# Optimization experiments

Measured on AMD Instinct MI355X. Metric: run time of the kernel, lower is better.

## Reference

```python
import jax, jax.numpy as jnp
import numpy as np

B, S, H = 2, 2048, 2048
NH, NKV, HD = 16, 4, 128
LAT = H // 8  # compression_ratio=8


def _rope_tables():
    inv_freq = 1.0 / (10000.0 ** (jnp.arange(0, HD, 2, dtype=jnp.float32) / HD))
    pos = jnp.arange(S, dtype=jnp.float32)
    freqs = pos[:, None] * inv_freq[None, :]          # [S, HD/2]
    emb = jnp.concatenate([freqs, freqs], axis=-1)    # [S, HD]
    return jnp.cos(emb)[None, None], jnp.sin(emb)[None, None]  # [1,1,S,HD]


def setup_inputs() -> dict:
    key = jax.random.key(0)
    ks = jax.random.split(key, 8)
    std = 0.02
    hidden_states = jax.random.normal(ks[0], (B, S, H), dtype=jnp.float32)
    cos, sin = _rope_tables()
    # additive causal mask, broadcast over batch/heads
    causal = jnp.tril(jnp.ones((S, S), dtype=bool))
    attention_mask = jnp.where(causal, 0.0, -1e9).astype(jnp.float32)[None, None]
    Wq = jax.random.normal(ks[1], (H, H), dtype=jnp.float32) * std
    Wk = jax.random.normal(ks[2], (NKV * HD, H), dtype=jnp.float32) * std
    Wv = jax.random.normal(ks[3], (NKV * HD, H), dtype=jnp.float32) * std
    Wo = jax.random.normal(ks[4], (H, H), dtype=jnp.float32) * std
    Wl_in = jax.random.normal(ks[5], (LAT, H), dtype=jnp.float32) * std
    Wl_out = jax.random.normal(ks[6], (H, LAT), dtype=jnp.float32) * std
    latent_gate = jnp.ones((1,), dtype=jnp.float32)
    return dict(hidden_states=hidden_states, cos=cos, sin=sin,
                attention_mask=attention_mask, Wq=Wq, Wk=Wk, Wv=Wv, Wo=Wo,
                Wl_in=Wl_in, Wl_out=Wl_out, latent_gate=latent_gate)


def _rotate_half(x):
    x1, x2 = jnp.split(x, 2, axis=-1)
    return jnp.concatenate([-x2, x1], axis=-1)


def reference(hidden_states, cos, sin, attention_mask, Wq, Wk, Wv, Wo,
              Wl_in, Wl_out, latent_gate):
    b, s, h = hidden_states.shape
    # projections (torch Linear: x @ W.T)
    q = (hidden_states @ Wq.T).reshape(b, s, NH, HD).transpose(0, 2, 1, 3)    # [b,nh,s,hd]
    k = (hidden_states @ Wk.T).reshape(b, s, NKV, HD).transpose(0, 2, 1, 3)   # [b,nkv,s,hd]
    v = (hidden_states @ Wv.T).reshape(b, s, NKV, HD).transpose(0, 2, 1, 3)
    # inline RoPE
    c, sn = cos[:, :, :s, :], sin[:, :, :s, :]
    q = q * c + _rotate_half(q) * sn
    k = k * c + _rotate_half(k) * sn
    # GQA: replicate kv heads (repeat_interleave along head dim)
    rep = NH // NKV
    k = jnp.repeat(k, rep, axis=1)
    v = jnp.repeat(v, rep, axis=1)
    scores = jnp.einsum('bhqd,bhkd->bhqk', q, k) / np.sqrt(HD).astype(np.float32)
    scores = scores + attention_mask
    attn = jax.nn.softmax(scores, axis=-1)
    ctx = jnp.einsum('bhqk,bhkd->bhqd', attn, v)          # [b,nh,s,hd]
    ctx = ctx.transpose(0, 2, 1, 3).reshape(b, s, h)
    attn_out = ctx @ Wo.T
    latent = (hidden_states @ Wl_in.T) @ Wl_out.T          # low-rank residual branch
    return attn_out + latent_gate * latent
```

## Files before the change

### kernel.cpp

```cpp
#include <hip/hip_runtime.h>
#include <hip/hip_bf16.h>

#define Bn   2
#define Sn   2048
#define Hn   2048
#define NHn  16
#define NKVn 4
#define HDn  128
#define LATn 256
#define Mn   (Bn*Sn)
#define KC   2304
#define NWn  3328

typedef unsigned short ushort_t;
typedef __attribute__((ext_vector_type(8))) short bf16x8;
typedef __attribute__((ext_vector_type(8))) unsigned short ushort8;
typedef __attribute__((ext_vector_type(4))) float f32x4;
typedef __attribute__((ext_vector_type(4))) unsigned u32x4;

__device__ __forceinline__ ushort_t f2bf(float f) {
    unsigned u = __float_as_uint(f);
    u += 0x7fffu + ((u >> 16) & 1u);
    return (ushort_t)(u >> 16);
}
__device__ __forceinline__ float bf2f(ushort_t h) {
    return __uint_as_float(((unsigned)h) << 16);
}
__device__ __forceinline__ unsigned cvt_pk_bf16(float lo, float hi) {
    unsigned r;
    asm("v_cvt_pk_bf16_f32 %0, %1, %2" : "=v"(r) : "v"(lo), "v"(hi));
    return r;
}
__device__ __forceinline__ void async16(const void* g, void* l) {
    __builtin_amdgcn_global_load_lds(
        (__attribute__((address_space(1))) void*)g,
        (__attribute__((address_space(3))) void*)l, 16, 0, 0);
}

struct CastArgs {
    const float* src[7];
    ushort_t*    dst[7];
    int n4[7];
    int sshift[7];
    int dcols[7];
    int dcoff[7];
};
__global__ __launch_bounds__(256)
void cast_fused(CastArgs a)
{
    int off = blockIdx.x * 256 + threadIdx.x;
    int seg = 0;
    while (seg < 6 && off >= a.n4[seg]) { off -= a.n4[seg]; ++seg; }
    const int r = off >> a.sshift[seg];
    const int c = off & ((1 << a.sshift[seg]) - 1);
    float4 f = ((const float4*)a.src[seg])[off];
    ushort4 o;
    o.x = f2bf(f.x); o.y = f2bf(f.y); o.z = f2bf(f.z); o.w = f2bf(f.w);
    ((ushort4*)a.dst[seg])[(size_t)r * a.dcols[seg] + a.dcoff[seg] + c] = o;
}

#define GEMM_BK64_LOOP(Aptr, Astr, Wptr, Wstr, Kdim)                          \
    for (int k0 = 0; k0 < (Kdim); k0 += 64) {                                 \
        _Pragma("unroll")                                                     \
        for (int it = 0; it < 4; ++it)                                        \
            async16((Aptr) + (size_t)(m0 + it*32 + srow)*(Astr) + k0 + scol,  \
                    As + (it*256 + tid)*8);                                   \
        _Pragma("unroll")                                                     \
        for (int it = 0; it < 4; ++it)                                        \
            async16((Wptr) + (size_t)(n0 + it*32 + srow)*(Wstr) + k0 + scol,  \
                    Bsm + (it*256 + tid)*8);                                  \
        __syncthreads();                                                      \
        _Pragma("unroll")                                                     \
        for (int hf = 0; hf < 2; ++hf) {                                      \
            bf16x8 af[4], bfr[4];                                             \
            _Pragma("unroll")                                                 \
            for (int mi = 0; mi < 4; ++mi)                                    \
                af[mi] = *(const bf16x8*)(As + aoff[hf*4 + mi]);              \
            _Pragma("unroll")                                                 \
            for (int ni = 0; ni < 4; ++ni)                                    \
                bfr[ni] = *(const bf16x8*)(Bsm + boff[hf*4 + ni]);            \
            _Pragma("unroll")                                                 \
            for (int mi = 0; mi < 4; ++mi)                                    \
                _Pragma("unroll")                                             \
                for (int ni = 0; ni < 4; ++ni)                                \
                    acc[mi][ni] = __builtin_amdgcn_mfma_f32_16x16x32_bf16(    \
                        af[mi], bfr[ni], acc[mi][ni], 0, 0, 0);               \
        }                                                                     \
        __syncthreads();                                                      \
    }

#define GEMM_COMMON_DECLS                                                     \
    const int tid  = threadIdx.x;                                             \
    const int lane = tid & 63, w = tid >> 6;                                  \
    const int t = lane & 15, q = lane >> 4;                                   \
    const int wm = w & 1, wn = w >> 1;                                        \
    const int srow = tid >> 3;                                                \
    const int scol = ((tid & 7) ^ ((tid >> 3) & 7)) * 8;                      \
    int aoff[8], boff[8];                                                     \
    _Pragma("unroll")                                                         \
    for (int hf = 0; hf < 2; ++hf)                                            \
        _Pragma("unroll")                                                     \
        for (int i = 0; i < 4; ++i) {                                         \
            aoff[hf*4 + i] = (wm*64 + i*16 + t)*64 + (((hf*4 + q) ^ (t & 7)) << 3); \
            boff[hf*4 + i] = (wn*64 + i*16 + t)*64 + (((hf*4 + q) ^ (t & 7)) << 3); \
        }                                                                     \
    f32x4 acc[4][4];                                                          \
    _Pragma("unroll")                                                         \
    for (int i = 0; i < 4; ++i)                                               \
        _Pragma("unroll")                                                     \
        for (int j = 0; j < 4; ++j) acc[i][j] = (f32x4){0.f, 0.f, 0.f, 0.f};

__global__ __launch_bounds__(256, 4)
void gemm_qkv(const ushort_t* __restrict__ A, const ushort_t* __restrict__ W,
              ushort_t* __restrict__ qo, ushort_t* __restrict__ ko,
              ushort_t* __restrict__ vo, ushort_t* __restrict__ ctxb,
              const float* __restrict__ gatep,
              const float* __restrict__ cosb, const float* __restrict__ sinb)
{
    __shared__ __align__(16) ushort_t smem[16384];
    ushort_t* As  = smem;
    ushort_t* Bsm = smem + 8192;

    const int m0 = blockIdx.y * 128, n0 = blockIdx.x * 128;
    GEMM_COMMON_DECLS
    GEMM_BK64_LOOP(A, Hn, W, Hn, Hn)

    const int bidx = m0 >> 11, s0 = m0 & (Sn - 1);

    if (n0 >= 2560 && n0 < 3072) {
        const int head = (n0 - 2560) >> 7;
        ushort_t* T = smem;
        #pragma unroll
        for (int h2 = 0; h2 < 2; ++h2) {
            __syncthreads();
            if (wn == h2) {
                #pragma unroll
                for (int mi = 0; mi < 4; ++mi)
                    #pragma unroll
                    for (int ni = 0; ni < 4; ++ni)
                        #pragma unroll
                        for (int r = 0; r < 4; ++r)
                            T[(wm*64 + mi*16 + q*4 + r)*64 + ni*16 + t] =
                                f2bf(acc[mi][ni][r]);
            }
            __syncthreads();
            const int dl = tid >> 2, tseg = (tid & 3) * 32;
            const size_t base =
                ((size_t)(bidx*NKVn + head)*HDn + h2*64 + dl) * Sn + s0 + tseg;
            #pragma unroll
            for (int j0 = 0; j0 < 4; ++j0) {
                ushort8 pk;
                #pragma unroll
                for (int u = 0; u < 8; ++u) {
                    const int p  = j0*8 + u;
                    const int qg = (p >> 3) & 3, j = p & 7;
                    const int orig = (j < 4) ? qg*4 + j : 16 + qg*4 + (j - 4);
                    pk[u] = T[(tseg + orig)*64 + dl];
                }
                *(ushort8*)(vo + base + j0*8) = pk;
            }
        }
        return;
    }

    if (n0 >= 3072) {
        const float gate = gatep[0];
        ushort_t* obase = ctxb + (size_t)m0 * KC + (2048 + (n0 - 3072));
        #pragma unroll
        for (int mi = 0; mi < 4; ++mi)
            #pragma unroll
            for (int r = 0; r < 4; ++r) {
                const int sl = wm*64 + mi*16 + q*4 + r;
                #pragma unroll
                for (int ni = 0; ni < 4; ++ni) {
                    const int d = wn*64 + ni*16 + t;
                    obase[(size_t)sl*KC + d] = f2bf(gate * acc[mi][ni][r]);
                }
            }
        return;
    }

    ushort_t* obase;
    float qsc;
    if (n0 < 2048) {
        obase = qo + (((size_t)(bidx*NHn + (n0 >> 7)))*Sn + s0) * HDn;
        qsc = 0.12751744737492532f;
    } else {
        obase = ko + (((size_t)(bidx*NKVn + ((n0 - 2048) >> 7)))*Sn + s0) * HDn;
        qsc = 1.0f;
    }

    float* smf = (float*)smem;
    if (wn == 1) {
        #pragma unroll
        for (int mi = 0; mi < 4; ++mi)
            #pragma unroll
            for (int r = 0; r < 4; ++r) {
                const int sl = wm*64 + mi*16 + q*4 + r;
                #pragma unroll
                for (int ni = 0; ni < 4; ++ni)
                    smf[sl*64 + (((ni*16 + t) ^ (((sl >> 2) & 3) << 4)))] =
                        acc[mi][ni][r];
            }
    }
    __syncthreads();
    if (wn == 0) {
        #pragma unroll
        for (int mi = 0; mi < 4; ++mi)
            #pragma unroll
            for (int r = 0; r < 4; ++r) {
                const int sl = wm*64 + mi*16 + q*4 + r;
                const int s  = s0 + sl;
                #pragma unroll
                for (int ni = 0; ni < 4; ++ni) {
                    const int d = ni*16 + t;
                    const float c  = cosb[s*HDn + d];
                    const float sn = sinb[s*HDn + d];
                    const float x0 = acc[mi][ni][r];
                    const float x1 = smf[sl*64 + (d ^ (((sl >> 2) & 3) << 4))];
                    obase[(size_t)sl*HDn + d] = f2bf(qsc*(x0*c - x1*sn));
                }
            }
    }
    __syncthreads();
    if (wn == 0) {
        #pragma unroll
        for (int mi = 0; mi < 4; ++mi)
            #pragma unroll
            for (int r = 0; r < 4; ++r) {
                const int sl = wm*64 + mi*16 + q*4 + r;
                #pragma unroll
                for (int ni = 0; ni < 4; ++ni)
                    smf[sl*64 + (((ni*16 + t) ^ (((sl >> 2) & 3) << 4)))] =
                        acc[mi][ni][r];
            }
    }
    __syncthreads();
    if (wn == 1) {
        #pragma unroll
        for (int mi = 0; mi < 4; ++mi)
            #pragma unroll
            for (int r = 0; r < 4; ++r) {
                const int sl = wm*64 + mi*16 + q*4 + r;
                const int s  = s0 + sl;
                #pragma unroll
                for (int ni = 0; ni < 4; ++ni) {
                    const int dl = ni*16 + t;
                    const int d  = 64 + dl;
                    const float c  = cosb[s*HDn + d];
                    const float sn = sinb[s*HDn + d];
                    const float x1 = acc[mi][ni][r];
                    const float x0 = smf[sl*64 + (dl ^ (((sl >> 2) & 3) << 4))];
                    obase[(size_t)sl*HDn + d] = f2bf(qsc*(x1*c + x0*sn));
                }
            }
    }
}

__global__ __launch_bounds__(256, 4)
void gemm_out(const ushort_t* __restrict__ A, const ushort_t* __restrict__ W,
              float* __restrict__ outf)
{
    __shared__ __align__(16) ushort_t smem[16384];
    ushort_t* As  = smem;
    ushort_t* Bsm = smem + 8192;

    const int m0 = blockIdx.y * 128, n0 = blockIdx.x * 128;
    GEMM_COMMON_DECLS
    GEMM_BK64_LOOP(A, KC, W, KC, KC)

    #pragma unroll
    for (int mi = 0; mi < 4; ++mi)
        #pragma unroll
        for (int r = 0; r < 4; ++r) {
            const int m = m0 + wm*64 + mi*16 + q*4 + r;
            #pragma unroll
            for (int ni = 0; ni < 4; ++ni) {
                const int n = n0 + wn*64 + ni*16 + t;
                outf[(size_t)m * Hn + n] = acc[mi][ni][r];
            }
        }
}

__global__ __launch_bounds__(256)
void attn_mfma(const ushort_t* __restrict__ qg, const ushort_t* __restrict__ kg,
               const ushort_t* __restrict__ vtg, ushort_t* __restrict__ ctxb)
{
    __shared__ __align__(16) ushort_t Ks[2][8192];
    __shared__ __align__(16) ushort_t Vt[2][8192];

    const int tid = threadIdx.x;
    const int w = tid >> 6, lane = tid & 63;
    const int t = lane & 15, q = lane >> 4;
    const int bh = blockIdx.y;
    const int b = bh >> 4, h = bh & 15;
    const int kvh = h >> 2;
    const ushort_t* qhead  = qg  + ((size_t)(b*NHn  + h  ))*Sn*HDn;
    const ushort_t* khead  = kg  + ((size_t)(b*NKVn + kvh))*Sn*HDn;
    const ushort_t* vthead = vtg + ((size_t)(b*NKVn + kvh))*HDn*Sn;

    const int ksr = tid >> 4;
    const int ksb = (tid & 15) ^ (ksr & 15);
    const int vtr = tid >> 3;
    const int vtb = (tid & 7) ^ (vtr & 7);

    int bko[16], vto[16];
    #pragma unroll
    for (int nb = 0; nb < 4; ++nb)
        #pragma unroll
        for (int ks = 0; ks < 4; ++ks)
            bko[nb*4 + ks] = (nb*16 + t)*128 + (((ks*4 + q) ^ t) << 3);
    #pragma unroll
    for (int d2 = 0; d2 < 8; ++d2)
        #pragma unroll
        for (int ksp = 0; ksp < 2; ++ksp)
            vto[d2*2 + ksp] = (d2*16 + t)*64 + (((ksp*4 + q) ^ (t & 7)) << 3);

    for (int rep = 0; rep < 2; ++rep) {
        const int qt = rep ? (31 - (int)blockIdx.x) : (int)blockIdx.x;

        bf16x8 aq[4];
        #pragma unroll
        for (int ks = 0; ks < 4; ++ks)
            aq[ks] = *(const bf16x8*)(
                qhead + (size_t)(qt*64 + w*16 + t)*HDn + ks*32 + q*8);

        __syncthreads();
        #pragma unroll
        for (int it = 0; it < 4; ++it)
            async16(khead + (size_t)(it*16 + ksr)*HDn + ksb*8,
                    Ks[0] + it*2048 + tid*8);
        #pragma unroll
        for (int it = 0; it < 4; ++it)
            async16(vthead + (size_t)(it*32 + vtr)*Sn + vtb*8,
                    Vt[0] + it*2048 + tid*8);
        __syncthreads();

        float l_sum = 0.f;
        f32x4 O[8];
        #pragma unroll
        for (int d2 = 0; d2 < 8; ++d2) O[d2] = (f32x4){0.f, 0.f, 0.f, 0.f};

        for (int kt = 0; kt <= qt; ++kt) {
            const ushort_t* Kc = Ks[kt & 1];
            const ushort_t* Vc = Vt[kt & 1];

            if (kt < qt) {
                #pragma unroll
                for (int it = 0; it < 4; ++it)
                    async16(khead + (size_t)((kt+1)*64 + it*16 + ksr)*HDn + ksb*8,
                            Ks[(kt & 1) ^ 1] + it*2048 + tid*8);
                #pragma unroll
                for (int it = 0; it < 4; ++it)
                    async16(vthead + (size_t)(it*32 + vtr)*Sn + (kt+1)*64 + vtb*8,
                            Vt[(kt & 1) ^ 1] + it*2048 + tid*8);
            }

            f32x4 sc[4];
            __builtin_amdgcn_s_setprio(1);
            #pragma unroll
            for (int nb = 0; nb < 4; ++nb) {
                sc[nb] = (f32x4){0.f, 0.f, 0.f, 0.f};
                #pragma unroll
                for (int ks = 0; ks < 4; ++ks) {
                    bf16x8 bk = *(const bf16x8*)(Kc + bko[nb*4 + ks]);
                    sc[nb] = __builtin_amdgcn_mfma_f32_16x16x32_bf16(
                        bk, aq[ks], sc[nb], 0, 0, 0);
                }
            }
            __builtin_amdgcn_s_setprio(0);

            float ps[4][4];
            if (kt == qt) {
                const int qi = w*16 + t;
                #pragma unroll
                for (int nb = 0; nb < 4; ++nb)
                    #pragma unroll
                    for (int r = 0; r < 4; ++r) {
                        const int kj = nb*16 + q*4 + r;
                        ps[nb][r] = (kj <= qi) ? exp2f(sc[nb][r]) : 0.f;
                    }
            } else {
                #pragma unroll
                for (int nb = 0; nb < 4; ++nb)
                    #pragma unroll
                    for (int r = 0; r < 4; ++r)
                        ps[nb][r] = exp2f(sc[nb][r]);
            }
            {
                float t0 = (ps[0][0] + ps[0][1]) + (ps[0][2] + ps[0][3]);
                float t1 = (ps[1][0] + ps[1][1]) + (ps[1][2] + ps[1][3]);
                float t2 = (ps[2][0] + ps[2][1]) + (ps[2][2] + ps[2][3]);
                float t3 = (ps[3][0] + ps[3][1]) + (ps[3][2] + ps[3][3]);
                l_sum += (t0 + t1) + (t2 + t3);
            }

            u32x4 pw0, pw1;
            pw0[0] = cvt_pk_bf16(ps[0][0], ps[0][1]);
            pw0[1] = cvt_pk_bf16(ps[0][2], ps[0][3]);
            pw0[2] = cvt_pk_bf16(ps[1][0], ps[1][1]);
            pw0[3] = cvt_pk_bf16(ps[1][2], ps[1][3]);
            pw1[0] = cvt_pk_bf16(ps[2][0], ps[2][1]);
            pw1[1] = cvt_pk_bf16(ps[2][2], ps[2][3]);
            pw1[2] = cvt_pk_bf16(ps[3][0], ps[3][1]);
            pw1[3] = cvt_pk_bf16(ps[3][2], ps[3][3]);
            const bf16x8 pa0 = __builtin_bit_cast(bf16x8, pw0);
            const bf16x8 pa1 = __builtin_bit_cast(bf16x8, pw1);

            __builtin_amdgcn_s_setprio(1);
            #pragma unroll
            for (int d2 = 0; d2 < 8; ++d2) {
                bf16x8 bv0 = *(const bf16x8*)(Vc + vto[d2*2 + 0]);
                O[d2] = __builtin_amdgcn_mfma_f32_16x16x32_bf16(pa0, bv0, O[d2], 0, 0, 0);
                bf16x8 bv1 = *(const bf16x8*)(Vc + vto[d2*2 + 1]);
                O[d2] = __builtin_amdgcn_mfma_f32_16x16x32_bf16(pa1, bv1, O[d2], 0, 0, 0);
            }
            __builtin_amdgcn_s_setprio(0);

            __syncthreads();
        }

        float lr = l_sum;
        lr += __shfl_xor(lr, 16);
        lr += __shfl_xor(lr, 32);
        float linv[4];
        #pragma unroll
        for (int r = 0; r < 4; ++r)
            linv[r] = 1.f / __shfl(lr, q*4 + r, 16);

        #pragma unroll
        for (int d2 = 0; d2 < 8; ++d2)
            #pragma unroll
            for (int r = 0; r < 4; ++r) {
                const size_t addr =
                    ((size_t)(b*Sn + qt*64 + w*16 + q*4 + r))*KC + h*HDn + d2*16 + t;
                ctxb[addr] = f2bf(O[d2][r] * linv[r]);
            }
    }
}

extern "C" void kernel_launch(void* const* d_in, const int* in_sizes, int n_in,
                              void* d_out, int out_size, void* d_ws, size_t ws_size,
                              hipStream_t stream)
{
    const float* hs    = (const float*)d_in[0];
    const float* cosb  = (const float*)d_in[1];
    const float* sinb  = (const float*)d_in[2];
    const float* Wq    = (const float*)d_in[4];
    const float* Wk    = (const float*)d_in[5];
    const float* Wv    = (const float*)d_in[6];
    const float* Wo    = (const float*)d_in[7];
    const float* Wlin  = (const float*)d_in[8];
    const float* Wlout = (const float*)d_in[9];
    const float* gate  = (const float*)d_in[10];
    float* out = (float*)d_out;

    ushort_t* p = (ushort_t*)d_ws;
    ushort_t* hsb    = p;  p += 8388608;
    ushort_t* Wqkvb  = p;  p += (size_t)NWn*2048;
    ushort_t* Wcomb  = p;  p += 2048*KC;
    ushort_t* qbb    = p;  p += 8388608;
    ushort_t* kbb    = p;  p += 2097152;
    ushort_t* vtb    = p;  p += 2097152;
    ushort_t* ctxc   = p;  p += (size_t)Mn*KC;

    const dim3 blk(256);

    {
        CastArgs ca;
        ca.src[0]=hs;    ca.dst[0]=hsb;                 ca.n4[0]=2097152; ca.sshift[0]=21; ca.dcols[0]=1<<21; ca.dcoff[0]=0;
        ca.src[1]=Wq;    ca.dst[1]=Wqkvb;               ca.n4[1]=1048576; ca.sshift[1]=20; ca.dcols[1]=1<<20; ca.dcoff[1]=0;
        ca.src[2]=Wk;    ca.dst[2]=Wqkvb + 2048*2048;   ca.n4[2]=262144;  ca.sshift[2]=18; ca.dcols[2]=1<<18; ca.dcoff[2]=0;
        ca.src[3]=Wv;    ca.dst[3]=Wqkvb + 2560*2048;   ca.n4[3]=262144;  ca.sshift[3]=18; ca.dcols[3]=1<<18; ca.dcoff[3]=0;
        ca.src[4]=Wlin;  ca.dst[4]=Wqkvb + 3072*2048;   ca.n4[4]=131072;  ca.sshift[4]=17; ca.dcols[4]=1<<17; ca.dcoff[4]=0;
        ca.src[5]=Wo;    ca.dst[5]=Wcomb;               ca.n4[5]=1048576; ca.sshift[5]=9;  ca.dcols[5]=576;   ca.dcoff[5]=0;
        ca.src[6]=Wlout; ca.dst[6]=Wcomb;               ca.n4[6]=131072;  ca.sshift[6]=6;  ca.dcols[6]=576;   ca.dcoff[6]=512;
        cast_fused<<<19456, blk, 0, stream>>>(ca);
    }

    gemm_qkv<<<dim3(26, 32), blk, 0, stream>>>(hsb, Wqkvb, qbb, kbb, vtb, ctxc,
                                               gate, cosb, sinb);

    attn_mfma<<<dim3(16, Bn*NHn), blk, 0, stream>>>(qbb, kbb, vtb, ctxc);

    gemm_out<<<dim3(16, 32), blk, 0, stream>>>(ctxc, Wcomb, out);
}
```

Before: 319.9 us.

## Load V fragments straight from global into registers, dropping V shared-memory staging

The attention kernel stops staging the transposed V tile in LDS. Each lane now loads its V MFMA operands directly from global memory into double-buffered register arrays, prefetching the next tile during the PV MFMAs. The loop is unrolled by two so the vA and vB buffers can ping-pong. This removes half the LDS traffic and footprint, but adds 32 bf16x8 registers per thread, which risks lower occupancy, and relies on uncoalesced-per-lane global loads hitting cache.

```diff
diff --git a/kernel.cpp b/kernel.cpp
--- a/kernel.cpp
+++ b/kernel.cpp
@@ -282,12 +282,89 @@
         }
 }
 
+#define ATTN_ITER(KT, VC, VN)                                                 \
+    {                                                                         \
+        const int kt_ = (KT);                                                 \
+        const ushort_t* Kc = Ks[kt_ & 1];                                     \
+        if (kt_ < qt) {                                                       \
+            _Pragma("unroll")                                                 \
+            for (int it = 0; it < 4; ++it)                                    \
+                async16(khead + (size_t)((kt_+1)*64 + it*16 + ksr)*HDn + ksb*8,\
+                        Ks[(kt_ & 1) ^ 1] + it*2048 + tid*8);                 \
+        }                                                                     \
+        f32x4 sc[4];                                                          \
+        __builtin_amdgcn_s_setprio(1);                                        \
+        _Pragma("unroll")                                                     \
+        for (int nb = 0; nb < 4; ++nb) {                                      \
+            sc[nb] = (f32x4){0.f, 0.f, 0.f, 0.f};                             \
+            _Pragma("unroll")                                                 \
+            for (int ks = 0; ks < 4; ++ks) {                                  \
+                bf16x8 bk = *(const bf16x8*)(Kc + bko[nb*4 + ks]);            \
+                sc[nb] = __builtin_amdgcn_mfma_f32_16x16x32_bf16(             \
+                    bk, aq[ks], sc[nb], 0, 0, 0);                             \
+            }                                                                 \
+        }                                                                     \
+        __builtin_amdgcn_s_setprio(0);                                        \
+        float ps[4][4];                                                       \
+        if (kt_ == qt) {                                                      \
+            const int qi = w*16 + t;                                          \
+            _Pragma("unroll")                                                 \
+            for (int nb = 0; nb < 4; ++nb)                                    \
+                _Pragma("unroll")                                             \
+                for (int r = 0; r < 4; ++r) {                                 \
+                    const int kj = nb*16 + q*4 + r;                           \
+                    ps[nb][r] = (kj <= qi) ? exp2f(sc[nb][r]) : 0.f;          \
+                }                                                             \
+        } else {                                                              \
+            _Pragma("unroll")                                                 \
+            for (int nb = 0; nb < 4; ++nb)                                    \
+                _Pragma("unroll")                                             \
+                for (int r = 0; r < 4; ++r)                                   \
+                    ps[nb][r] = exp2f(sc[nb][r]);                             \
+        }                                                                     \
+        {                                                                     \
+            float t0 = (ps[0][0] + ps[0][1]) + (ps[0][2] + ps[0][3]);         \
+            float t1 = (ps[1][0] + ps[1][1]) + (ps[1][2] + ps[1][3]);         \
+            float t2 = (ps[2][0] + ps[2][1]) + (ps[2][2] + ps[2][3]);         \
+            float t3 = (ps[3][0] + ps[3][1]) + (ps[3][2] + ps[3][3]);         \
+            l_sum += (t0 + t1) + (t2 + t3);                                   \
+        }                                                                     \
+        u32x4 pw0, pw1;                                                       \
+        pw0[0] = cvt_pk_bf16(ps[0][0], ps[0][1]);                             \
+        pw0[1] = cvt_pk_bf16(ps[0][2], ps[0][3]);                             \
+        pw0[2] = cvt_pk_bf16(ps[1][0], ps[1][1]);                             \
+        pw0[3] = cvt_pk_bf16(ps[1][2], ps[1][3]);                             \
+        pw1[0] = cvt_pk_bf16(ps[2][0], ps[2][1]);                             \
+        pw1[1] = cvt_pk_bf16(ps[2][2], ps[2][3]);                             \
+        pw1[2] = cvt_pk_bf16(ps[3][0], ps[3][1]);                             \
+        pw1[3] = cvt_pk_bf16(ps[3][2], ps[3][3]);                             \
+        const bf16x8 pa0 = __builtin_bit_cast(bf16x8, pw0);                   \
+        const bf16x8 pa1 = __builtin_bit_cast(bf16x8, pw1);                   \
+        const bool pf_ = (kt_ < qt);                                          \
+        const size_t vs_ = (size_t)(kt_ + 1) * 64;                            \
+        __builtin_amdgcn_s_setprio(1);                                        \
+        _Pragma("unroll")                                                     \
+        for (int d2 = 0; d2 < 8; ++d2) {                                      \
+            O[d2] = __builtin_amdgcn_mfma_f32_16x16x32_bf16(                  \
+                pa0, VC[d2*2 + 0], O[d2], 0, 0, 0);                           \
+            O[d2] = __builtin_amdgcn_mfma_f32_16x16x32_bf16(                  \
+                pa1, VC[d2*2 + 1], O[d2], 0, 0, 0);                           \
+            if (pf_) {                                                        \
+                VN[d2*2 + 0] = *(const bf16x8*)(                              \
+                    vthead + (size_t)(d2*16 + t)*Sn + vs_ + q*8);             \
+                VN[d2*2 + 1] = *(const bf16x8*)(                              \
+                    vthead + (size_t)(d2*16 + t)*Sn + vs_ + 32 + q*8);        \
+            }                                                                 \
+        }                                                                     \
+        __builtin_amdgcn_s_setprio(0);                                        \
+        __syncthreads();                                                      \
+    }
+
 __global__ __launch_bounds__(256)
 void attn_mfma(const ushort_t* __restrict__ qg, const ushort_t* __restrict__ kg,
                const ushort_t* __restrict__ vtg, ushort_t* __restrict__ ctxb)
 {
     __shared__ __align__(16) ushort_t Ks[2][8192];
-    __shared__ __align__(16) ushort_t Vt[2][8192];
 
     const int tid = threadIdx.x;
     const int w = tid >> 6, lane = tid & 63;
@@ -301,20 +378,13 @@
 
     const int ksr = tid >> 4;
     const int ksb = (tid & 15) ^ (ksr & 15);
-    const int vtr = tid >> 3;
-    const int vtb = (tid & 7) ^ (vtr & 7);
-
-    int bko[16], vto[16];
+
+    int bko[16];
     #pragma unroll
     for (int nb = 0; nb < 4; ++nb)
         #pragma unroll
         for (int ks = 0; ks < 4; ++ks)
             bko[nb*4 + ks] = (nb*16 + t)*128 + (((ks*4 + q) ^ t) << 3);
-    #pragma unroll
-    for (int d2 = 0; d2 < 8; ++d2)
-        #pragma unroll
-        for (int ksp = 0; ksp < 2; ++ksp)
-            vto[d2*2 + ksp] = (d2*16 + t)*64 + (((ksp*4 + q) ^ (t & 7)) << 3);
 
     for (int rep = 0; rep < 2; ++rep) {
         const int qt = rep ? (31 - (int)blockIdx.x) : (int)blockIdx.x;
@@ -325,15 +395,20 @@
             aq[ks] = *(const bf16x8*)(
                 qhead + (size_t)(qt*64 + w*16 + t)*HDn + ks*32 + q*8);
 
+        bf16x8 vA[16], vB[16];
+        #pragma unroll
+        for (int d2 = 0; d2 < 8; ++d2) {
+            vA[d2*2 + 0] = *(const bf16x8*)(
+                vthead + (size_t)(d2*16 + t)*Sn + q*8);
+            vA[d2*2 + 1] = *(const bf16x8*)(
+                vthead + (size_t)(d2*16 + t)*Sn + 32 + q*8);
+        }
+
         __syncthreads();
         #pragma unroll
         for (int it = 0; it < 4; ++it)
             async16(khead + (size_t)(it*16 + ksr)*HDn + ksb*8,
                     Ks[0] + it*2048 + tid*8);
-        #pragma unroll
-        for (int it = 0; it < 4; ++it)
-            async16(vthead + (size_t)(it*32 + vtr)*Sn + vtb*8,
-                    Vt[0] + it*2048 + tid*8);
         __syncthreads();
 
         float l_sum = 0.f;
@@ -341,83 +416,9 @@
         #pragma unroll
         for (int d2 = 0; d2 < 8; ++d2) O[d2] = (f32x4){0.f, 0.f, 0.f, 0.f};
 
-        for (int kt = 0; kt <= qt; ++kt) {
-            const ushort_t* Kc = Ks[kt & 1];
-            const ushort_t* Vc = Vt[kt & 1];
-
-            if (kt < qt) {
-                #pragma unroll
-                for (int it = 0; it < 4; ++it)
-                    async16(khead + (size_t)((kt+1)*64 + it*16 + ksr)*HDn + ksb*8,
-                            Ks[(kt & 1) ^ 1] + it*2048 + tid*8);
-                #pragma unroll
-                for (int it = 0; it < 4; ++it)
-                    async16(vthead + (size_t)(it*32 + vtr)*Sn + (kt+1)*64 + vtb*8,
-                            Vt[(kt & 1) ^ 1] + it*2048 + tid*8);
-            }
-
-            f32x4 sc[4];
-            __builtin_amdgcn_s_setprio(1);
-            #pragma unroll
-            for (int nb = 0; nb < 4; ++nb) {
-                sc[nb] = (f32x4){0.f, 0.f, 0.f, 0.f};
-                #pragma unroll
-                for (int ks = 0; ks < 4; ++ks) {
-                    bf16x8 bk = *(const bf16x8*)(Kc + bko[nb*4 + ks]);
-                    sc[nb] = __builtin_amdgcn_mfma_f32_16x16x32_bf16(
-                        bk, aq[ks], sc[nb], 0, 0, 0);
-                }
-            }
-            __builtin_amdgcn_s_setprio(0);
-
-            float ps[4][4];
-            if (kt == qt) {
-                const int qi = w*16 + t;
-                #pragma unroll
-                for (int nb = 0; nb < 4; ++nb)
-                    #pragma unroll
-                    for (int r = 0; r < 4; ++r) {
-                        const int kj = nb*16 + q*4 + r;
-                        ps[nb][r] = (kj <= qi) ? exp2f(sc[nb][r]) : 0.f;
-                    }
-            } else {
-                #pragma unroll
-                for (int nb = 0; nb < 4; ++nb)
-                    #pragma unroll
-                    for (int r = 0; r < 4; ++r)
-                        ps[nb][r] = exp2f(sc[nb][r]);
-            }
-            {
-                float t0 = (ps[0][0] + ps[0][1]) + (ps[0][2] + ps[0][3]);
-                float t1 = (ps[1][0] + ps[1][1]) + (ps[1][2] + ps[1][3]);
-                float t2 = (ps[2][0] + ps[2][1]) + (ps[2][2] + ps[2][3]);
-                float t3 = (ps[3][0] + ps[3][1]) + (ps[3][2] + ps[3][3]);
-                l_sum += (t0 + t1) + (t2 + t3);
-            }
-
-            u32x4 pw0, pw1;
-            pw0[0] = cvt_pk_bf16(ps[0][0], ps[0][1]);
-            pw0[1] = cvt_pk_bf16(ps[0][2], ps[0][3]);
-            pw0[2] = cvt_pk_bf16(ps[1][0], ps[1][1]);
-            pw0[3] = cvt_pk_bf16(ps[1][2], ps[1][3]);
-            pw1[0] = cvt_pk_bf16(ps[2][0], ps[2][1]);
-            pw1[1] = cvt_pk_bf16(ps[2][2], ps[2][3]);
-            pw1[2] = cvt_pk_bf16(ps[3][0], ps[3][1]);
-            pw1[3] = cvt_pk_bf16(ps[3][2], ps[3][3]);
-            const bf16x8 pa0 = __builtin_bit_cast(bf16x8, pw0);
-            const bf16x8 pa1 = __builtin_bit_cast(bf16x8, pw1);
-
-            __builtin_amdgcn_s_setprio(1);
-            #pragma unroll
-            for (int d2 = 0; d2 < 8; ++d2) {
-                bf16x8 bv0 = *(const bf16x8*)(Vc + vto[d2*2 + 0]);
-                O[d2] = __builtin_amdgcn_mfma_f32_16x16x32_bf16(pa0, bv0, O[d2], 0, 0, 0);
-                bf16x8 bv1 = *(const bf16x8*)(Vc + vto[d2*2 + 1]);
-                O[d2] = __builtin_amdgcn_mfma_f32_16x16x32_bf16(pa1, bv1, O[d2], 0, 0, 0);
-            }
-            __builtin_amdgcn_s_setprio(0);
-
-            __syncthreads();
+        for (int kt = 0; kt <= qt; kt += 2) {
+            ATTN_ITER(kt, vA, vB)
+            if (kt + 1 <= qt) ATTN_ITER(kt + 1, vB, vA)
         }
 
         float lr = l_sum;
```

Measured after the change: 427.1 us. +33.5%, slower.
